# Optimization experiments

Measured on AMD Instinct MI355X. Metric: run time of the kernel, lower is better.

## Reference

```python
import jax, jax.numpy as jnp
import numpy as np

N_NODES = 100000
N_EDGES = 1600000
HID = 128
BOND = 16
BN_EPS = 1e-5


def setup_inputs() -> dict:
    key = jax.random.key(0)
    ks = jax.random.split(key, 12)
    sb = 1.0 / np.sqrt(BOND)
    sh = 1.0 / np.sqrt(HID)
    return {
        "features": jax.random.normal(ks[0], (N_NODES, HID), jnp.float32),
        "edge_feats": jax.random.normal(ks[1], (N_EDGES, BOND), jnp.float32),
        "src": jax.random.randint(ks[2], (N_EDGES,), 0, N_NODES, jnp.int32),
        "dst": jax.random.randint(ks[3], (N_EDGES,), 0, N_NODES, jnp.int32),
        "Wb": jax.random.uniform(ks[4], (HID, BOND), jnp.float32, -sb, sb),
        "bb": jax.random.uniform(ks[5], (HID,), jnp.float32, -sb, sb),
        "W1": jax.random.uniform(ks[6], (HID, HID), jnp.float32, -sh, sh),
        "b1": jax.random.uniform(ks[7], (HID,), jnp.float32, -sh, sh),
        "W2": jax.random.uniform(ks[8], (HID, HID), jnp.float32, -sh, sh),
        "b2": jax.random.uniform(ks[9], (HID,), jnp.float32, -sh, sh),
        "gamma1": jnp.ones((HID,), jnp.float32),
        "beta1": jnp.zeros((HID,), jnp.float32),
        "gamma2": jnp.ones((HID,), jnp.float32),
        "beta2": jnp.zeros((HID,), jnp.float32),
    }


def _batchnorm(x, gamma, beta):
    # BatchNorm1d in training mode: normalize with batch stats (biased var).
    mean = jnp.mean(x, axis=0)
    var = jnp.var(x, axis=0)
    return (x - mean) * jax.lax.rsqrt(var + BN_EPS) * gamma + beta


def reference(features, edge_feats, src, dst, Wb, bb, W1, b1, W2, b2,
              gamma1, beta1, gamma2, beta2):
    n = features.shape[0]
    # edge linear: [E, BOND] -> [E, HID]
    eh = edge_feats @ Wb.T + bb
    # mailbox sums: sum of src node features and edge messages per dst node
    h1 = jax.ops.segment_sum(features[src], dst, num_segments=n)  # [N, HID]
    h2 = jax.ops.segment_sum(eh, dst, num_segments=n)             # [N, HID]
    h = jax.nn.relu(_batchnorm(h1 @ W1.T + b1 + h2, gamma1, beta1))
    h = jax.nn.relu(_batchnorm(h @ W2.T + b2 + features, gamma2, beta2))
    return h
```

## Files before the change

kernel.cpp:

```cpp
#include <hip/hip_runtime.h>

#define NN 100000
#define NE 1600000
#define HID 128
#define KEXT 160
#define ROWB 320
#define BSH 9
#define BNODES 512
#define NB 196
#define P2B 256
#define EPB2 6250
#define T2 2048
#define SCAP 10240
#define NROWP 100096
#define GGRID 782
#define BN_EPS 1e-5f

typedef __attribute__((ext_vector_type(8))) short bf16x8;
typedef __attribute__((ext_vector_type(4))) float f32x4;

__device__ inline unsigned short f2bf(float x) {
  union { float f; unsigned u; } v; v.f = x;
  unsigned r = v.u + 0x7FFFu + ((v.u >> 16) & 1u);
  return (unsigned short)(r >> 16);
}
__device__ inline unsigned pk2(float a, float b) {
  return (unsigned)f2bf(a) | ((unsigned)f2bf(b) << 16);
}
__device__ inline float bflo(unsigned p) { return __uint_as_float(p << 16); }
__device__ inline float bfhi(unsigned p) { return __uint_as_float(p & 0xffff0000u); }

__device__ inline void gload_lds16(const void* g, void* l) {
  __builtin_amdgcn_global_load_lds((const __attribute__((address_space(1))) void*)g,
                                   (__attribute__((address_space(3))) void*)l, 16, 0, 0);
}

__global__ __launch_bounds__(256) void fbw_k(const float* __restrict__ f,
                                             unsigned* __restrict__ fb,
                                             const float* __restrict__ W1,
                                             const float* __restrict__ Wb,
                                             const float* __restrict__ bb,
                                             const float* __restrict__ b1,
                                             const float* __restrict__ W2,
                                             unsigned short* __restrict__ W1e,
                                             unsigned short* __restrict__ W2e,
                                             const int* __restrict__ dst,
                                             int* __restrict__ cnts_s) {
  __shared__ int bh[NB];
  if (blockIdx.x < 25000) {
    int i = blockIdx.x * 256 + threadIdx.x;
    float2 v = ((const float2*)f)[i];
    fb[i] = pk2(v.x, v.y);
  } else if (blockIdx.x < 25080) {
    int idx = (blockIdx.x - 25000) * 256 + threadIdx.x;
    if (idx < 128 * KEXT) {
      int c = idx / KEXT, k = idx - c * KEXT;
      float v1 = 0.f;
      if (k < 128) v1 = W1[c * HID + k];
      else if (k < 144) v1 = Wb[c * 16 + (k - 128)];
      else if (k == 144) v1 = bb[c];
      else if (k == 145) v1 = b1[c];
      W1e[idx] = f2bf(v1);
    }
    if (idx < 128 * 128) W2e[idx] = f2bf(W2[(idx >> 7) * HID + (idx & 127)]);
  } else {
    int blk = blockIdx.x - 25080;
    int b0 = blk * EPB2, e1 = b0 + EPB2;
    for (int i = threadIdx.x; i < NB; i += 256) bh[i] = 0;
    __syncthreads();
    for (int e = b0 + threadIdx.x; e < e1; e += 256) atomicAdd(&bh[dst[e] >> BSH], 1);
    __syncthreads();
    for (int i = threadIdx.x; i < NB; i += 256) cnts_s[i * P2B + blk] = bh[i];
  }
}

__global__ __launch_bounds__(P2B) void cscan_k(int* __restrict__ cnts_s,
                                               int* __restrict__ bcnt_s,
                                               int* __restrict__ bcnt_r) {
  __shared__ int s[P2B];
  int b = blockIdx.x, t = threadIdx.x;
  int x = cnts_s[b * P2B + t];
  int xs = (x + 7) & ~7;
  s[t] = xs; __syncthreads();
  for (int off = 1; off < P2B; off <<= 1) {
    int v = (t >= off) ? s[t - off] : 0; __syncthreads();
    s[t] += v; __syncthreads();
  }
  cnts_s[b * P2B + t] = s[t] - xs;
  if (t == P2B - 1) bcnt_s[b] = s[t];
  __syncthreads();
  s[t] = x; __syncthreads();
  for (int off = 1; off < P2B; off <<= 1) {
    int v = (t >= off) ? s[t - off] : 0; __syncthreads();
    s[t] += v; __syncthreads();
  }
  if (t == P2B - 1) bcnt_r[b] = s[t];
}

__global__ __launch_bounds__(256) void bscan_k(const int* __restrict__ bcnt_r,
                                               const int* __restrict__ bcnt_s,
                                               int* __restrict__ bbase_r,
                                               int* __restrict__ bbase_s,
                                               int* __restrict__ rs) {
  __shared__ int s[256];
  int t = threadIdx.x;
#pragma unroll
  for (int pass = 0; pass < 2; ++pass) {
    const int* in = (pass == 0) ? bcnt_r : bcnt_s;
    int* out = (pass == 0) ? bbase_r : bbase_s;
    int x = (t < NB) ? in[t] : 0;
    s[t] = x; __syncthreads();
    for (int off = 1; off < 256; off <<= 1) {
      int v = (t >= off) ? s[t - off] : 0; __syncthreads();
      s[t] += v; __syncthreads();
    }
    if (t < NB) out[t] = s[t] - x;
    if (t == NB - 1) out[NB] = s[t];
    __syncthreads();
  }
  if (t == 0) rs[NN] = NE;
}

__global__ __launch_bounds__(1024) void part3_k(const int* __restrict__ src,
                                                const int* __restrict__ dst,
                                                const float* __restrict__ ef,
                                                const int* __restrict__ bbase_s,
                                                const int* __restrict__ cnts_s,
                                                unsigned* __restrict__ stg,
                                                float4* __restrict__ efb) {
  __shared__ int th[NB], ts[NB], cnt2[NB], run[NB], st_s[NB];
  __shared__ int sscan[256];
  __shared__ unsigned spk[T2];
  __shared__ float4 eflds[T2 * 2];
  int blk = blockIdx.x, tid = threadIdx.x;
  int b0 = blk * EPB2, e1 = b0 + EPB2;
  for (int i = tid; i < NB; i += 1024) {
    run[i] = 0;
    st_s[i] = bbase_s[i] + cnts_s[i * P2B + blk];
  }
  for (int t0 = b0; t0 < e1; t0 += T2) {
    int tc = min(T2, e1 - t0);
    for (int i = tid; i < NB; i += 1024) { th[i] = 0; cnt2[i] = 0; }
    __syncthreads();
    for (int le = tid; le < tc; le += 1024) {
      int e = t0 + le;
      atomicAdd(&th[dst[e] >> BSH], 1);
      const float4* efp = (const float4*)(ef + (size_t)e * 16);
      float4 e0 = efp[0], e1v = efp[1], e2 = efp[2], e3 = efp[3];
      float4 w0, w1;
      w0.x = __uint_as_float(pk2(e0.x, e0.y));  w0.y = __uint_as_float(pk2(e0.z, e0.w));
      w0.z = __uint_as_float(pk2(e1v.x, e1v.y)); w0.w = __uint_as_float(pk2(e1v.z, e1v.w));
      w1.x = __uint_as_float(pk2(e2.x, e2.y));  w1.y = __uint_as_float(pk2(e2.z, e2.w));
      w1.z = __uint_as_float(pk2(e3.x, e3.y));  w1.w = __uint_as_float(pk2(e3.z, e3.w));
      eflds[le * 2] = w0;
      eflds[le * 2 + 1] = w1;
    }
    __syncthreads();
    if (tid < 256) sscan[tid] = (tid < NB) ? th[tid] : 0;
    __syncthreads();
    for (int off = 1; off < 256; off <<= 1) {
      int v = 0;
      if (tid < 256 && tid >= off) v = sscan[tid - off];
      __syncthreads();
      if (tid < 256) sscan[tid] += v;
      __syncthreads();
    }
    if (tid < NB) ts[tid] = sscan[tid] - th[tid];
    __syncthreads();
    for (int le = tid; le < tc; le += 1024) {
      int b = dst[t0 + le] >> BSH;
      int slot = ts[b] + atomicAdd(&cnt2[b], 1);
      spk[slot] = ((unsigned)b << 11) | (unsigned)le;
    }
    __syncthreads();
    for (int s2 = tid; s2 < tc; s2 += 1024) {
      unsigned pk = spk[s2];
      int b = pk >> 11, le = pk & 2047;
      int e = t0 + le;
      int gs = st_s[b] + run[b] + (s2 - ts[b]);
      int d9 = dst[e] & (BNODES - 1);
      stg[gs] = (unsigned)src[e] | ((unsigned)d9 << 17) | (1u << 26);
      efb[(size_t)gs * 2] = eflds[le * 2];
      efb[(size_t)gs * 2 + 1] = eflds[le * 2 + 1];
    }
    __syncthreads();
    for (int i = tid; i < NB; i += 1024) run[i] += th[i];
    __syncthreads();
  }
  for (int i = tid; i < NB; i += 1024) {
    int c = run[i];
    int cs = (c + 7) & ~7;
    for (int j = c; j < cs; ++j) stg[st_s[i] + j] = 0u;
  }
}

__global__ __launch_bounds__(512) void bsort_k(const unsigned* __restrict__ stg,
                                               const int* __restrict__ bbase_s,
                                               const int* __restrict__ bbase_r,
                                               const unsigned* __restrict__ efbu,
                                               int* __restrict__ rs,
                                               unsigned* __restrict__ fin,
                                               unsigned* __restrict__ efsum) {
  __shared__ int h[BNODES], sc[BNODES], cur[BNODES];
  __shared__ int tot;
  __shared__ unsigned slds[SCAP];
  int b = blockIdx.x, n0 = b << BSH, tid = threadIdx.x;
  int s0p = bbase_s[b], e1p = bbase_s[b + 1];
  int s0r = bbase_r[b];
  h[tid] = 0;
  __syncthreads();
  for (int i = s0p + tid; i < e1p; i += 512) {
    unsigned rec = stg[i];
    if (rec >> 26) atomicAdd(&h[(rec >> 17) & (BNODES - 1)], 1);
  }
  __syncthreads();
  sc[tid] = h[tid];
  __syncthreads();
  for (int off = 1; off < BNODES; off <<= 1) {
    int v = (tid >= off) ? sc[tid - off] : 0;
    __syncthreads();
    sc[tid] += v;
    __syncthreads();
  }
  int excl = sc[tid] - h[tid];
  cur[tid] = excl;
  int n = n0 + tid;
  if (n < NN) rs[n] = s0r + excl;
  if (tid == BNODES - 1) tot = sc[tid];
  __syncthreads();
  for (int i = s0p + tid; i < e1p; i += 512) {
    unsigned rec = stg[i];
    if (rec >> 26) {
      int d = (rec >> 17) & (BNODES - 1);
      int p = atomicAdd(&cur[d], 1);
      slds[p] = (rec & 0x1FFFF) | ((unsigned)(i - s0p) << 17);
    }
  }
  __syncthreads();
  int T = tot;
  for (int j = tid; j < T; j += 512) fin[s0r + j] = slds[j] & 0x1FFFF;
  if (n < NN) {
    float a[16];
#pragma unroll
    for (int k = 0; k < 16; ++k) a[k] = 0.f;
    for (int j = excl; j < sc[tid]; ++j) {
      unsigned rec = slds[j];
      const unsigned* ep = efbu + ((size_t)s0p + (rec >> 17)) * 8;
#pragma unroll
      for (int k = 0; k < 8; ++k) {
        unsigned u = ep[k];
        a[2 * k] += bflo(u);
        a[2 * k + 1] += bfhi(u);
      }
    }
    unsigned* op = efsum + (size_t)n * 8;
#pragma unroll
    for (int k = 0; k < 8; ++k) op[k] = pk2(a[2 * k], a[2 * k + 1]);
  }
}

__global__ __launch_bounds__(256) void feg_k(const unsigned* __restrict__ fb,
                                             const int* __restrict__ rs,
                                             const unsigned* __restrict__ fin,
                                             const unsigned* __restrict__ efsum,
                                             unsigned short* __restrict__ A1) {
  int bid = (int)(blockIdx.x & 7) * 3125 + (int)(blockIdx.x >> 3);
  int wid = threadIdx.x >> 6, lane = threadIdx.x & 63;
  int node = bid * 4 + wid;
  if (node >= NN) return;
  int start = rs[node], end = rs[node + 1];
  float ax0 = 0.f, ay0 = 0.f, ax1 = 0.f, ay1 = 0.f;
  float ax2 = 0.f, ay2 = 0.f, ax3 = 0.f, ay3 = 0.f;
  float ax4 = 0.f, ay4 = 0.f, ax5 = 0.f, ay5 = 0.f;
  float ax6 = 0.f, ay6 = 0.f, ax7 = 0.f, ay7 = 0.f;
  int i = start;
  for (; i + 8 <= end; i += 8) {
    int sl = 0;
    if (lane < 8) sl = (int)fin[i + lane];
    int s0 = __shfl(sl, 0), s1 = __shfl(sl, 1), s2 = __shfl(sl, 2), s3 = __shfl(sl, 3);
    int s4 = __shfl(sl, 4), s5 = __shfl(sl, 5), s6 = __shfl(sl, 6), s7 = __shfl(sl, 7);
    unsigned p0 = fb[s0 * 64 + lane];
    unsigned p1 = fb[s1 * 64 + lane];
    unsigned p2 = fb[s2 * 64 + lane];
    unsigned p3 = fb[s3 * 64 + lane];
    unsigned p4 = fb[s4 * 64 + lane];
    unsigned p5 = fb[s5 * 64 + lane];
    unsigned p6 = fb[s6 * 64 + lane];
    unsigned p7 = fb[s7 * 64 + lane];
    ax0 += bflo(p0); ay0 += bfhi(p0);
    ax1 += bflo(p1); ay1 += bfhi(p1);
    ax2 += bflo(p2); ay2 += bfhi(p2);
    ax3 += bflo(p3); ay3 += bfhi(p3);
    ax4 += bflo(p4); ay4 += bfhi(p4);
    ax5 += bflo(p5); ay5 += bfhi(p5);
    ax6 += bflo(p6); ay6 += bfhi(p6);
    ax7 += bflo(p7); ay7 += bfhi(p7);
  }
  for (; i < end; ++i) {
    int sl = 0;
    if (lane == 0) sl = (int)fin[i];
    int s0 = __shfl(sl, 0);
    unsigned p0 = fb[s0 * 64 + lane];
    ax0 += bflo(p0); ay0 += bfhi(p0);
  }
  float ax = ((ax0 + ax1) + (ax2 + ax3)) + ((ax4 + ax5) + (ax6 + ax7));
  float ay = ((ay0 + ay1) + (ay2 + ay3)) + ((ay4 + ay5) + (ay6 + ay7));
  char* rowp = (char*)A1 + (size_t)node * ROWB;
  *(unsigned*)(rowp + lane * 4) = pk2(ax, ay);
  if (lane < 8) {
    *(unsigned*)(rowp + 256 + 4 * lane) = efsum[(size_t)node * 8 + lane];
  } else if (lane < 16) {
    int j2 = lane - 8;
    *(unsigned*)(rowp + 288 + 4 * j2) =
        (j2 == 0) ? pk2((float)(end - start), 1.0f) : 0u;
  }
}

__global__ __launch_bounds__(256) void gemm1_k(
    const unsigned short* __restrict__ A, const unsigned short* __restrict__ W,
    unsigned short* __restrict__ outb, float* __restrict__ statsP) {
  __shared__ __align__(16) char sA[128 * ROWB];
  __shared__ __align__(16) char sW[128 * ROWB];
  const int tid = threadIdx.x;
  const int wid = tid >> 6, lane = tid & 63;
  const size_t r0 = (size_t)blockIdx.x * 128;

#pragma unroll
  for (int q = 0; q < 10; ++q) {
    int s = q * 256 + tid;
    int row = (s * 3277) >> 16;
    int c = s - row * 20;
    int csrc = (c < 16) ? (c ^ (row & 7)) : (16 + ((c - 16) ^ (row & 3)));
    gload_lds16((const char*)A + (r0 + row) * ROWB + csrc * 16,
                sA + (size_t)(q * 256 + wid * 64) * 16);
  }
#pragma unroll
  for (int q = 0; q < 10; ++q) {
    int s = q * 256 + tid;
    int row = (s * 3277) >> 16;
    int c = s - row * 20;
    int csrc = (c < 16) ? (c ^ (row & 7)) : (16 + ((c - 16) ^ (row & 3)));
    gload_lds16((const char*)W + (size_t)row * ROWB + csrc * 16,
                sW + (size_t)(q * 256 + wid * 64) * 16);
  }
  __syncthreads();

  const int l15 = lane & 15;
  const int kgr = lane >> 4;
  bf16x8 afrag[2][5];
#pragma unroll
  for (int rt = 0; rt < 2; ++rt) {
    int arow = wid * 32 + rt * 16 + l15;
#pragma unroll
    for (int ks = 0; ks < 5; ++ks) {
      int creq = ks * 4 + kgr;
      int csw = (creq < 16) ? (creq ^ (arow & 7)) : (16 + ((creq - 16) ^ (arow & 3)));
      afrag[rt][ks] = *(const bf16x8*)(sA + arow * ROWB + csw * 16);
    }
  }
  f32x4 acc[2][8];
#pragma unroll
  for (int rt = 0; rt < 2; ++rt)
#pragma unroll
    for (int ct = 0; ct < 8; ++ct) acc[rt][ct] = (f32x4){0.f, 0.f, 0.f, 0.f};
#pragma unroll
  for (int ct = 0; ct < 8; ++ct) {
    int brow = ct * 16 + l15;
#pragma unroll
    for (int ks = 0; ks < 5; ++ks) {
      int creq = ks * 4 + kgr;
      int csw = (creq < 16) ? (creq ^ (brow & 7)) : (16 + ((creq - 16) ^ (brow & 3)));
      bf16x8 bfrag = *(const bf16x8*)(sW + brow * ROWB + csw * 16);
      acc[0][ct] = __builtin_amdgcn_mfma_f32_16x16x32_bf16(afrag[0][ks], bfrag, acc[0][ct], 0, 0, 0);
      acc[1][ct] = __builtin_amdgcn_mfma_f32_16x16x32_bf16(afrag[1][ks], bfrag, acc[1][ct], 0, 0, 0);
    }
  }

  float cs[8], cq[8];
#pragma unroll
  for (int ct = 0; ct < 8; ++ct) { cs[ct] = 0.f; cq[ct] = 0.f; }
#pragma unroll
  for (int rt = 0; rt < 2; ++rt) {
    const size_t orow0 = r0 + wid * 32 + rt * 16 + kgr * 4;
#pragma unroll
    for (int ct = 0; ct < 8; ++ct) {
      int col = ct * 16 + l15;
#pragma unroll
      for (int r = 0; r < 4; ++r) {
        size_t row = orow0 + r;
        if (row < NN) {
          float v = acc[rt][ct][r];
          outb[row * HID + col] = f2bf(v);
          cs[ct] += v; cq[ct] += v * v;
        }
      }
    }
  }
#pragma unroll
  for (int ct = 0; ct < 8; ++ct) {
    cs[ct] += __shfl_xor(cs[ct], 16); cs[ct] += __shfl_xor(cs[ct], 32);
    cq[ct] += __shfl_xor(cq[ct], 16); cq[ct] += __shfl_xor(cq[ct], 32);
  }
  __syncthreads();
  float* red = (float*)sA;
  if (lane < 16) {
#pragma unroll
    for (int ct = 0; ct < 8; ++ct) {
      red[wid * 256 + ct * 16 + l15] = cs[ct];
      red[wid * 256 + 128 + ct * 16 + l15] = cq[ct];
    }
  }
  __syncthreads();
  if (tid < 256) {
    float* base = statsP + (size_t)(blockIdx.x & 15) * 512;
    float s_ = red[tid] + red[256 + tid] + red[512 + tid] + red[768 + tid];
    atomicAdd(&base[tid], s_);
  }
}

__global__ void bnred_k(const float* __restrict__ statsP, int base,
                        const float* __restrict__ gamma, const float* __restrict__ beta,
                        float* __restrict__ scale, float* __restrict__ shift) {
  int c = threadIdx.x;
  if (c < 128) {
    float s_ = 0.f, q_ = 0.f;
#pragma unroll
    for (int i = 0; i < 16; ++i) {
      s_ += statsP[i * 512 + base + c];
      q_ += statsP[i * 512 + base + 128 + c];
    }
    const float invN = 1.f / (float)NN;
    float m = s_ * invN;
    float var = q_ * invN - m * m;
    float inv = rsqrtf(var + BN_EPS);
    float sc = gamma[c] * inv;
    scale[c] = sc;
    shift[c] = beta[c] - m * sc;
  }
}

__global__ __launch_bounds__(256) void gemm2_k(
    const unsigned* __restrict__ t, const unsigned short* __restrict__ W,
    const float* __restrict__ scale, const float* __restrict__ shift,
    const float* __restrict__ b2, const float* __restrict__ F,
    unsigned short* __restrict__ outb, float* __restrict__ statsP) {
  __shared__ __align__(16) char sA[128 * 256];
  __shared__ __align__(16) char sW[128 * 256];
  __shared__ float ssc[128], ssh[128];
  const int tid = threadIdx.x;
  const int wid = tid >> 6, lane = tid & 63;
  const size_t r0 = (size_t)blockIdx.x * 128;

  if (tid < 128) {
    ssc[tid] = scale[tid];
    ssh[tid] = shift[tid];
  }
#pragma unroll
  for (int q = 0; q < 8; ++q) {
    int s = q * 256 + tid;
    int row = s >> 4, c = s & 15;
    int csrc = c ^ (row & 7);
    gload_lds16((const char*)W + (size_t)row * 256 + csrc * 16,
                sW + (size_t)(q * 256 + wid * 64) * 16);
  }
  __syncthreads();

#pragma unroll
  for (int q = 0; q < 8; ++q) {
    int s = q * 256 + tid;
    int sr = s >> 4, c = s & 15;
    size_t grow = r0 + sr;
    uint4 v = make_uint4(0, 0, 0, 0);
    if (grow < NN) v = *(const uint4*)(t + grow * 64 + c * 4);
    int k = c * 8;
    unsigned o0 = pk2(fmaxf(0.f, fmaf(bflo(v.x), ssc[k + 0], ssh[k + 0])),
                      fmaxf(0.f, fmaf(bfhi(v.x), ssc[k + 1], ssh[k + 1])));
    unsigned o1 = pk2(fmaxf(0.f, fmaf(bflo(v.y), ssc[k + 2], ssh[k + 2])),
                      fmaxf(0.f, fmaf(bfhi(v.y), ssc[k + 3], ssh[k + 3])));
    unsigned o2 = pk2(fmaxf(0.f, fmaf(bflo(v.z), ssc[k + 4], ssh[k + 4])),
                      fmaxf(0.f, fmaf(bfhi(v.z), ssc[k + 5], ssh[k + 5])));
    unsigned o3 = pk2(fmaxf(0.f, fmaf(bflo(v.w), ssc[k + 6], ssh[k + 6])),
                      fmaxf(0.f, fmaf(bfhi(v.w), ssc[k + 7], ssh[k + 7])));
    int csw = c ^ (sr & 7);
    uint4 w4; w4.x = o0; w4.y = o1; w4.z = o2; w4.w = o3;
    *(uint4*)(sA + sr * 256 + csw * 16) = w4;
  }
  __syncthreads();

  const int l15 = lane & 15;
  const int kgr = lane >> 4;
  bf16x8 afrag[2][4];
#pragma unroll
  for (int rt = 0; rt < 2; ++rt) {
    int arow = wid * 32 + rt * 16 + l15;
#pragma unroll
    for (int ks = 0; ks < 4; ++ks) {
      int creq = ks * 4 + kgr;
      int csw = creq ^ (arow & 7);
      afrag[rt][ks] = *(const bf16x8*)(sA + arow * 256 + csw * 16);
    }
  }
  f32x4 acc[2][8];
#pragma unroll
  for (int rt = 0; rt < 2; ++rt)
#pragma unroll
    for (int ct = 0; ct < 8; ++ct) acc[rt][ct] = (f32x4){0.f, 0.f, 0.f, 0.f};
#pragma unroll
  for (int ct = 0; ct < 8; ++ct) {
    int brow = ct * 16 + l15;
#pragma unroll
    for (int ks = 0; ks < 4; ++ks) {
      int creq = ks * 4 + kgr;
      int csw = creq ^ (brow & 7);
      bf16x8 bfrag = *(const bf16x8*)(sW + brow * 256 + csw * 16);
      acc[0][ct] = __builtin_amdgcn_mfma_f32_16x16x32_bf16(afrag[0][ks], bfrag, acc[0][ct], 0, 0, 0);
      acc[1][ct] = __builtin_amdgcn_mfma_f32_16x16x32_bf16(afrag[1][ks], bfrag, acc[1][ct], 0, 0, 0);
    }
  }

  float cs[8], cq[8];
#pragma unroll
  for (int ct = 0; ct < 8; ++ct) { cs[ct] = 0.f; cq[ct] = 0.f; }
#pragma unroll
  for (int rt = 0; rt < 2; ++rt) {
    const size_t orow0 = r0 + wid * 32 + rt * 16 + kgr * 4;
#pragma unroll
    for (int ct = 0; ct < 8; ++ct) {
      int col = ct * 16 + l15;
      float b2v = b2[col];
#pragma unroll
      for (int r = 0; r < 4; ++r) {
        size_t row = orow0 + r;
        if (row < NN) {
          float v = acc[rt][ct][r] + b2v + F[row * HID + col];
          outb[row * HID + col] = f2bf(v);
          cs[ct] += v; cq[ct] += v * v;
        }
      }
    }
  }
#pragma unroll
  for (int ct = 0; ct < 8; ++ct) {
    cs[ct] += __shfl_xor(cs[ct], 16); cs[ct] += __shfl_xor(cs[ct], 32);
    cq[ct] += __shfl_xor(cq[ct], 16); cq[ct] += __shfl_xor(cq[ct], 32);
  }
  __syncthreads();
  float* red = (float*)sA;
  if (lane < 16) {
#pragma unroll
    for (int ct = 0; ct < 8; ++ct) {
      red[wid * 256 + ct * 16 + l15] = cs[ct];
      red[wid * 256 + 128 + ct * 16 + l15] = cq[ct];
    }
  }
  __syncthreads();
  if (tid < 256) {
    float* base = statsP + (size_t)(blockIdx.x & 15) * 512 + 256;
    float s_ = red[tid] + red[256 + tid] + red[512 + tid] + red[768 + tid];
    atomicAdd(&base[tid], s_);
  }
}

__global__ __launch_bounds__(256) void bn_final_k(const unsigned* __restrict__ t,
                                                  const float* __restrict__ scale,
                                                  const float* __restrict__ shift,
                                                  float* __restrict__ o) {
  __shared__ float ssc[128], ssh[128];
  int tid = threadIdx.x;
  if (tid < 128) { ssc[tid] = scale[tid]; ssh[tid] = shift[tid]; }
  __syncthreads();
  int i = blockIdx.x * 256 + tid;
  if (i >= NN * 64) return;
  unsigned p = t[i];
  int c = (i & 63) * 2;
  float2 v;
  v.x = fmaxf(0.f, fmaf(bflo(p), ssc[c], ssh[c]));
  v.y = fmaxf(0.f, fmaf(bfhi(p), ssc[c + 1], ssh[c + 1]));
  ((float2*)o)[i] = v;
}

extern "C" void kernel_launch(void* const* d_in, const int* in_sizes, int n_in,
                              void* d_out, int out_size, void* d_ws, size_t ws_size,
                              hipStream_t stream) {
  (void)in_sizes; (void)n_in; (void)out_size; (void)ws_size;
  const float* features   = (const float*)d_in[0];
  const float* edge_feats = (const float*)d_in[1];
  const int*   src        = (const int*)d_in[2];
  const int*   dst        = (const int*)d_in[3];
  const float* Wb         = (const float*)d_in[4];
  const float* bb         = (const float*)d_in[5];
  const float* W1         = (const float*)d_in[6];
  const float* b1         = (const float*)d_in[7];
  const float* W2         = (const float*)d_in[8];
  const float* b2         = (const float*)d_in[9];
  const float* gamma1     = (const float*)d_in[10];
  const float* beta1      = (const float*)d_in[11];
  const float* gamma2     = (const float*)d_in[12];
  const float* beta2      = (const float*)d_in[13];
  float* outp = (float*)d_out;

  char* wsb = (char*)d_ws;
  size_t off = 0;
  auto alloc = [&](size_t nbytes) -> void* {
    off = (off + 255) & ~(size_t)255;
    void* p = wsb + off;
    off += nbytes;
    return p;
  };
  const size_t STGN = (size_t)NE + 7 * NB * P2B + 64;
  int* row_start = (int*)alloc((size_t)(NN + 1) * 4);
  int* bcnt_r    = (int*)alloc(NB * 4);
  int* bcnt_s    = (int*)alloc(NB * 4);
  int* bbase_r   = (int*)alloc((NB + 1) * 4);
  int* bbase_s   = (int*)alloc((NB + 1) * 4);
  int* cnts_s    = (int*)alloc((size_t)NB * P2B * 4);
  float* statsP  = (float*)alloc(16 * 512 * 4);
  float* scsh    = (float*)alloc(512 * 4);
  unsigned* featb = (unsigned*)alloc((size_t)NROWP * 64 * 4);
  unsigned short* A1e = (unsigned short*)alloc((size_t)NROWP * ROWB);
  unsigned short* W1e = (unsigned short*)alloc(128 * KEXT * 2);
  unsigned short* W2e = (unsigned short*)alloc(128 * 128 * 2);
  unsigned* stg  = (unsigned*)alloc(STGN * 4);
  unsigned* fin  = (unsigned*)alloc((size_t)NE * 4);
  float4* efb    = (float4*)alloc(STGN * 32);
  unsigned* efsum = (unsigned*)alloc((size_t)NN * 32);
  unsigned short* tbuf = (unsigned short*)featb;

  hipMemsetAsync(statsP, 0, 16 * 512 * 4, stream);
  hipMemsetAsync((char*)A1e + (size_t)NN * ROWB, 0, (NROWP - NN) * ROWB, stream);
  hipMemsetAsync((char*)featb + (size_t)NN * 256, 0, (NROWP - NN) * 256, stream);

  fbw_k<<<25336, 256, 0, stream>>>(features, featb, W1, Wb, bb, b1, W2, W1e, W2e,
                                   dst, cnts_s);
  cscan_k<<<NB, P2B, 0, stream>>>(cnts_s, bcnt_s, bcnt_r);
  bscan_k<<<1, 256, 0, stream>>>(bcnt_r, bcnt_s, bbase_r, bbase_s, row_start);
  part3_k<<<P2B, 1024, 0, stream>>>(src, dst, edge_feats, bbase_s, cnts_s, stg, efb);
  bsort_k<<<NB, 512, 0, stream>>>(stg, bbase_s, bbase_r, (const unsigned*)efb,
                                  row_start, fin, efsum);
  feg_k<<<25000, 256, 0, stream>>>(featb, row_start, fin, efsum, A1e);

  gemm1_k<<<GGRID, 256, 0, stream>>>(A1e, W1e, tbuf, statsP);
  bnred_k<<<1, 128, 0, stream>>>(statsP, 0, gamma1, beta1, scsh, scsh + 128);
  gemm2_k<<<GGRID, 256, 0, stream>>>((const unsigned*)tbuf, W2e, scsh, scsh + 128,
                                     b2, features, tbuf, statsP);
  bnred_k<<<1, 128, 0, stream>>>(statsP, 256, gamma2, beta2, scsh + 256, scsh + 384);
  bn_final_k<<<25000, 256, 0, stream>>>((const unsigned*)tbuf, scsh + 256, scsh + 384,
                                        outp);
}
```

Measured before the change: 304.1 us.

## Restructure edge partitioning, LDS edge-feature reduction, and bf16 residual read

Result: slower. 451.1 us (+48.4%).

```diff
diff --git a/kernel.cpp b/kernel.cpp
--- a/kernel.cpp
+++ b/kernel.cpp
@@ -8,9 +8,8 @@
 #define BSH 9
 #define BNODES 512
 #define NB 196
-#define P2B 256
-#define EPB2 6250
-#define T2 2048
+#define P2B 1024
+#define EPB2 1563
 #define SCAP 10240
 #define NROWP 100096
 #define GGRID 782
@@ -65,7 +64,7 @@
     if (idx < 128 * 128) W2e[idx] = f2bf(W2[(idx >> 7) * HID + (idx & 127)]);
   } else {
     int blk = blockIdx.x - 25080;
-    int b0 = blk * EPB2, e1 = b0 + EPB2;
+    int b0 = blk * EPB2, e1 = min(b0 + EPB2, NE);
     for (int i = threadIdx.x; i < NB; i += 256) bh[i] = 0;
     __syncthreads();
     for (int e = b0 + threadIdx.x; e < e1; e += 256) atomicAdd(&bh[dst[e] >> BSH], 1);
@@ -121,74 +120,70 @@
   if (t == 0) rs[NN] = NE;
 }
 
-__global__ __launch_bounds__(1024) void part3_k(const int* __restrict__ src,
-                                                const int* __restrict__ dst,
-                                                const float* __restrict__ ef,
-                                                const int* __restrict__ bbase_s,
-                                                const int* __restrict__ cnts_s,
-                                                unsigned* __restrict__ stg,
-                                                float4* __restrict__ efb) {
-  __shared__ int th[NB], ts[NB], cnt2[NB], run[NB], st_s[NB];
+__global__ __launch_bounds__(256) void part3_k(const int* __restrict__ src,
+                                               const int* __restrict__ dst,
+                                               const float* __restrict__ ef,
+                                               const int* __restrict__ bbase_s,
+                                               const int* __restrict__ cnts_s,
+                                               unsigned* __restrict__ stg,
+                                               float4* __restrict__ efb) {
+  __shared__ int th[NB], ts[NB], cnt2[NB], st_s[NB];
   __shared__ int sscan[256];
-  __shared__ unsigned spk[T2];
-  __shared__ float4 eflds[T2 * 2];
+  __shared__ unsigned spk[EPB2 + 1];
   int blk = blockIdx.x, tid = threadIdx.x;
-  int b0 = blk * EPB2, e1 = b0 + EPB2;
-  for (int i = tid; i < NB; i += 1024) {
-    run[i] = 0;
+  int b0 = blk * EPB2;
+  int tc = min(EPB2, NE - b0);
+  for (int i = tid; i < NB; i += 256) {
+    th[i] = 0; cnt2[i] = 0;
     st_s[i] = bbase_s[i] + cnts_s[i * P2B + blk];
   }
-  for (int t0 = b0; t0 < e1; t0 += T2) {
-    int tc = min(T2, e1 - t0);
-    for (int i = tid; i < NB; i += 1024) { th[i] = 0; cnt2[i] = 0; }
+  __syncthreads();
+  float sink = 0.f;
+  for (int le = tid; le < tc; le += 256) {
+    int e = b0 + le;
+    atomicAdd(&th[dst[e] >> BSH], 1);
+    const float4* efp = (const float4*)(ef + (size_t)e * 16);
+    float4 a = efp[0], b4 = efp[1], c4 = efp[2], d4 = efp[3];
+    sink += a.x + b4.x + c4.x + d4.x;
+  }
+  asm volatile("" : "+v"(sink));
+  __syncthreads();
+  sscan[tid] = (tid < NB) ? th[tid] : 0;
+  __syncthreads();
+  for (int off = 1; off < 256; off <<= 1) {
+    int v = (tid >= off) ? sscan[tid - off] : 0;
     __syncthreads();
-    for (int le = tid; le < tc; le += 1024) {
-      int e = t0 + le;
-      atomicAdd(&th[dst[e] >> BSH], 1);
-      const float4* efp = (const float4*)(ef + (size_t)e * 16);
-      float4 e0 = efp[0], e1v = efp[1], e2 = efp[2], e3 = efp[3];
-      float4 w0, w1;
-      w0.x = __uint_as_float(pk2(e0.x, e0.y));  w0.y = __uint_as_float(pk2(e0.z, e0.w));
-      w0.z = __uint_as_float(pk2(e1v.x, e1v.y)); w0.w = __uint_as_float(pk2(e1v.z, e1v.w));
-      w1.x = __uint_as_float(pk2(e2.x, e2.y));  w1.y = __uint_as_float(pk2(e2.z, e2.w));
-      w1.z = __uint_as_float(pk2(e3.x, e3.y));  w1.w = __uint_as_float(pk2(e3.z, e3.w));
-      eflds[le * 2] = w0;
-      eflds[le * 2 + 1] = w1;
-    }
+    sscan[tid] += v;
     __syncthreads();
-    if (tid < 256) sscan[tid] = (tid < NB) ? th[tid] : 0;
-    __syncthreads();
-    for (int off = 1; off < 256; off <<= 1) {
-      int v = 0;
-      if (tid < 256 && tid >= off) v = sscan[tid - off];
-      __syncthreads();
-      if (tid < 256) sscan[tid] += v;
-      __syncthreads();
-    }
-    if (tid < NB) ts[tid] = sscan[tid] - th[tid];
-    __syncthreads();
-    for (int le = tid; le < tc; le += 1024) {
-      int b = dst[t0 + le] >> BSH;
-      int slot = ts[b] + atomicAdd(&cnt2[b], 1);
-      spk[slot] = ((unsigned)b << 11) | (unsigned)le;
-    }
-    __syncthreads();
-    for (int s2 = tid; s2 < tc; s2 += 1024) {
-      unsigned pk = spk[s2];
-      int b = pk >> 11, le = pk & 2047;
-      int e = t0 + le;
-      int gs = st_s[b] + run[b] + (s2 - ts[b]);
-      int d9 = dst[e] & (BNODES - 1);
-      stg[gs] = (unsigned)src[e] | ((unsigned)d9 << 17) | (1u << 26);
-      efb[(size_t)gs * 2] = eflds[le * 2];
-      efb[(size_t)gs * 2 + 1] = eflds[le * 2 + 1];
-    }
-    __syncthreads();
-    for (int i = tid; i < NB; i += 1024) run[i] += th[i];
-    __syncthreads();
-  }
-  for (int i = tid; i < NB; i += 1024) {
-    int c = run[i];
+  }
+  if (tid < NB) ts[tid] = sscan[tid] - th[tid];
+  __syncthreads();
+  for (int le = tid; le < tc; le += 256) {
+    int d = dst[b0 + le];
+    int b = d >> BSH;
+    int slot = ts[b] + atomicAdd(&cnt2[b], 1);
+    spk[slot] = ((unsigned)b << 20) | ((unsigned)(d & (BNODES - 1)) << 11) | (unsigned)le;
+  }
+  __syncthreads();
+  for (int s2 = tid; s2 < tc; s2 += 256) {
+    unsigned pk = spk[s2];
+    int b = pk >> 20, d9 = (pk >> 11) & 511, le = pk & 2047;
+    int e = b0 + le;
+    int gs = st_s[b] + (s2 - ts[b]);
+    stg[gs] = (unsigned)src[e] | ((unsigned)d9 << 17) | (1u << 26);
+    const float4* efp = (const float4*)(ef + (size_t)e * 16);
+    float4 a = efp[0], b4 = efp[1], c4 = efp[2], d4 = efp[3];
+    float4 w0, w1;
+    w0.x = __uint_as_float(pk2(a.x, a.y));   w0.y = __uint_as_float(pk2(a.z, a.w));
+    w0.z = __uint_as_float(pk2(b4.x, b4.y)); w0.w = __uint_as_float(pk2(b4.z, b4.w));
+    w1.x = __uint_as_float(pk2(c4.x, c4.y)); w1.y = __uint_as_float(pk2(c4.z, c4.w));
+    w1.z = __uint_as_float(pk2(d4.x, d4.y)); w1.w = __uint_as_float(pk2(d4.z, d4.w));
+    efb[(size_t)gs * 2] = w0;
+    efb[(size_t)gs * 2 + 1] = w1;
+  }
+  __syncthreads();
+  for (int i = tid; i < NB; i += 256) {
+    int c = th[i];
     int cs = (c + 7) & ~7;
     for (int j = c; j < cs; ++j) stg[st_s[i] + j] = 0u;
   }
@@ -203,11 +198,13 @@
                                                unsigned* __restrict__ efsum) {
   __shared__ int h[BNODES], sc[BNODES], cur[BNODES];
   __shared__ int tot;
-  __shared__ unsigned slds[SCAP];
+  __shared__ __align__(16) unsigned pool[SCAP];
+  float* efl = (float*)pool;
   int b = blockIdx.x, n0 = b << BSH, tid = threadIdx.x;
   int s0p = bbase_s[b], e1p = bbase_s[b + 1];
   int s0r = bbase_r[b];
   h[tid] = 0;
+  for (int j = tid; j < BNODES * 16; j += 512) efl[j] = 0.f;
   __syncthreads();
   for (int i = s0p + tid; i < e1p; i += 512) {
     unsigned rec = stg[i];
@@ -232,31 +229,33 @@
     unsigned rec = stg[i];
     if (rec >> 26) {
       int d = (rec >> 17) & (BNODES - 1);
-      int p = atomicAdd(&cur[d], 1);
-      slds[p] = (rec & 0x1FFFF) | ((unsigned)(i - s0p) << 17);
-    }
-  }
-  __syncthreads();
-  int T = tot;
-  for (int j = tid; j < T; j += 512) fin[s0r + j] = slds[j] & 0x1FFFF;
-  if (n < NN) {
-    float a[16];
-#pragma unroll
-    for (int k = 0; k < 16; ++k) a[k] = 0.f;
-    for (int j = excl; j < sc[tid]; ++j) {
-      unsigned rec = slds[j];
-      const unsigned* ep = efbu + ((size_t)s0p + (rec >> 17)) * 8;
+      const unsigned* ep = efbu + (size_t)i * 8;
 #pragma unroll
       for (int k = 0; k < 8; ++k) {
         unsigned u = ep[k];
-        a[2 * k] += bflo(u);
-        a[2 * k + 1] += bfhi(u);
+        atomicAdd(&efl[d * 16 + 2 * k], bflo(u));
+        atomicAdd(&efl[d * 16 + 2 * k + 1], bfhi(u));
       }
     }
-    unsigned* op = efsum + (size_t)n * 8;
-#pragma unroll
-    for (int k = 0; k < 8; ++k) op[k] = pk2(a[2 * k], a[2 * k + 1]);
-  }
+  }
+  __syncthreads();
+  for (int m = tid; m < BNODES * 8; m += 512) {
+    int n2 = m >> 3, k = m & 7;
+    if (n0 + n2 < NN)
+      efsum[(size_t)(n0 + n2) * 8 + k] = pk2(efl[n2 * 16 + 2 * k], efl[n2 * 16 + 2 * k + 1]);
+  }
+  __syncthreads();
+  for (int i = s0p + tid; i < e1p; i += 512) {
+    unsigned rec = stg[i];
+    if (rec >> 26) {
+      int d = (rec >> 17) & (BNODES - 1);
+      int p = atomicAdd(&cur[d], 1);
+      pool[p] = rec & 0x1FFFF;
+    }
+  }
+  __syncthreads();
+  int T = tot;
+  for (int j = tid; j < T; j += 512) fin[s0r + j] = pool[j];
 }
 
 __global__ __launch_bounds__(256) void feg_k(const unsigned* __restrict__ fb,
@@ -442,7 +441,7 @@
 __global__ __launch_bounds__(256) void gemm2_k(
     const unsigned* __restrict__ t, const unsigned short* __restrict__ W,
     const float* __restrict__ scale, const float* __restrict__ shift,
-    const float* __restrict__ b2, const float* __restrict__ F,
+    const float* __restrict__ b2, const unsigned* __restrict__ fbres,
     unsigned short* __restrict__ outb, float* __restrict__ statsP) {
   __shared__ __align__(16) char sA[128 * 256];
   __shared__ __align__(16) char sW[128 * 256];
@@ -528,11 +527,14 @@
     for (int ct = 0; ct < 8; ++ct) {
       int col = ct * 16 + l15;
       float b2v = b2[col];
+      int ci = col >> 1, par = col & 1;
 #pragma unroll
       for (int r = 0; r < 4; ++r) {
         size_t row = orow0 + r;
         if (row < NN) {
-          float v = acc[rt][ct][r] + b2v + F[row * HID + col];
+          unsigned u = fbres[row * 64 + ci];
+          float resid = par ? bfhi(u) : bflo(u);
+          float v = acc[rt][ct][r] + b2v + resid;
           outb[row * HID + col] = f2bf(v);
           cs[ct] += v; cq[ct] += v * v;
         }
@@ -607,7 +609,7 @@
     off += nbytes;
     return p;
   };
-  const size_t STGN = (size_t)NE + 7 * NB * P2B + 64;
+  const size_t STGN = (size_t)NE + 7 * (size_t)NB * P2B + 64;
   int* row_start = (int*)alloc((size_t)(NN + 1) * 4);
   int* bcnt_r    = (int*)alloc(NB * 4);
   int* bcnt_s    = (int*)alloc(NB * 4);
@@ -616,7 +618,8 @@
   int* cnts_s    = (int*)alloc((size_t)NB * P2B * 4);
   float* statsP  = (float*)alloc(16 * 512 * 4);
   float* scsh    = (float*)alloc(512 * 4);
-  unsigned* featb = (unsigned*)alloc((size_t)NROWP * 64 * 4);
+  unsigned* featb = (unsigned*)alloc((size_t)NN * 64 * 4);
+  unsigned short* tbuf = (unsigned short*)alloc((size_t)NROWP * HID * 2);
   unsigned short* A1e = (unsigned short*)alloc((size_t)NROWP * ROWB);
   unsigned short* W1e = (unsigned short*)alloc(128 * KEXT * 2);
   unsigned short* W2e = (unsigned short*)alloc(128 * 128 * 2);
@@ -624,17 +627,15 @@
   unsigned* fin  = (unsigned*)alloc((size_t)NE * 4);
   float4* efb    = (float4*)alloc(STGN * 32);
   unsigned* efsum = (unsigned*)alloc((size_t)NN * 32);
-  unsigned short* tbuf = (unsigned short*)featb;
 
   hipMemsetAsync(statsP, 0, 16 * 512 * 4, stream);
   hipMemsetAsync((char*)A1e + (size_t)NN * ROWB, 0, (NROWP - NN) * ROWB, stream);
-  hipMemsetAsync((char*)featb + (size_t)NN * 256, 0, (NROWP - NN) * 256, stream);
-
-  fbw_k<<<25336, 256, 0, stream>>>(features, featb, W1, Wb, bb, b1, W2, W1e, W2e,
-                                   dst, cnts_s);
+
+  fbw_k<<<25080 + P2B, 256, 0, stream>>>(features, featb, W1, Wb, bb, b1, W2,
+                                         W1e, W2e, dst, cnts_s);
   cscan_k<<<NB, P2B, 0, stream>>>(cnts_s, bcnt_s, bcnt_r);
   bscan_k<<<1, 256, 0, stream>>>(bcnt_r, bcnt_s, bbase_r, bbase_s, row_start);
-  part3_k<<<P2B, 1024, 0, stream>>>(src, dst, edge_feats, bbase_s, cnts_s, stg, efb);
+  part3_k<<<P2B, 256, 0, stream>>>(src, dst, edge_feats, bbase_s, cnts_s, stg, efb);
   bsort_k<<<NB, 512, 0, stream>>>(stg, bbase_s, bbase_r, (const unsigned*)efb,
                                   row_start, fin, efsum);
   feg_k<<<25000, 256, 0, stream>>>(featb, row_start, fin, efsum, A1e);
@@ -642,7 +643,7 @@
   gemm1_k<<<GGRID, 256, 0, stream>>>(A1e, W1e, tbuf, statsP);
   bnred_k<<<1, 128, 0, stream>>>(statsP, 0, gamma1, beta1, scsh, scsh + 128);
   gemm2_k<<<GGRID, 256, 0, stream>>>((const unsigned*)tbuf, W2e, scsh, scsh + 128,
-                                     b2, features, tbuf, statsP);
+                                     b2, featb, tbuf, statsP);
   bnred_k<<<1, 128, 0, stream>>>(statsP, 256, gamma2, beta2, scsh + 256, scsh + 384);
   bn_final_k<<<25000, 256, 0, stream>>>((const unsigned*)tbuf, scsh + 256, scsh + 384,
                                         outp);
```
